# Performance work log

Hardware: AMD Instinct MI355X
Metric: run time of the kernel (lower is better)

## Reference

```python
import jax, jax.numpy as jnp
import numpy as np

B, C, H, W = 16, 64, 64, 64
HEADS = 8

def conv1x1(x, w):
    # x: [B, Cin, H, W], w: [Cout, Cin] -> [B, Cout, H, W]
    return jnp.einsum('oc,bchw->bohw', w, x)

def maxpool2x2(x):
    b, c, h, w = x.shape
    return x.reshape(b, c, h // 2, 2, w // 2, 2).max(axis=(3, 5))

def setup_inputs() -> dict:
    key = jax.random.key(0)
    ks = jax.random.split(key, 6)
    x = jax.random.normal(ks[0], (B, C, H, W), dtype=jnp.float32)
    w_theta = jax.random.normal(ks[1], (C // HEADS, C), dtype=jnp.float32) * 0.05
    w_phi = jax.random.normal(ks[2], (C // HEADS, C), dtype=jnp.float32) * 0.05
    w_g = jax.random.normal(ks[3], (C // 2, C), dtype=jnp.float32) * 0.05
    w_o = jax.random.normal(ks[4], (C, C // 2), dtype=jnp.float32) * 0.05
    gamma = jax.random.normal(ks[5], (), dtype=jnp.float32)
    return {'x': x, 'w_theta': w_theta, 'w_phi': w_phi, 'w_g': w_g, 'w_o': w_o, 'gamma': gamma}

def reference(x, w_theta, w_phi, w_g, w_o, gamma):
    b, c, h, w = x.shape
    n = h * w                      # query length
    m = n // 4                     # kv length after 2x2 maxpool
    theta = conv1x1(x, w_theta).reshape(b, c // HEADS, n)   # [B, C/h, N]
    phi = maxpool2x2(conv1x1(x, w_phi)).reshape(b, c // HEADS, m)  # [B, C/h, M]
    g = maxpool2x2(conv1x1(x, w_g)).reshape(b, c // 2, m)   # [B, C/2, M]
    # attention: theta^T @ phi -> [B, N, M]; NOTE: no 1/sqrt(d) scaling (SAGAN)
    beta = jax.nn.softmax(jnp.einsum('bdn,bdm->bnm', theta, phi), axis=-1)
    # o = g @ beta^T -> [B, C/2, N]
    o = jnp.einsum('bdm,bnm->bdn', g, beta).reshape(b, c // 2, h, w)
    o = conv1x1(o, w_o)            # [B, C, H, W]
    return gamma * o + x
```

## Files before the change

kernel.cpp:

```cpp
#include <hip/hip_runtime.h>
#include <hip/hip_bf16.h>

#define NB 16
#define NC 64
#define NN 4096
#define NM 1024
#define ND 8
#define NG 32

typedef short short8 __attribute__((ext_vector_type(8)));
typedef float floatx4 __attribute__((ext_vector_type(4)));

#define LOG2E 1.44269504f

__device__ __forceinline__ short f2bfs(float f) {
    union { __hip_bfloat16 h; short s; } u;
    u.h = __float2bfloat16(f);
    return u.s;
}
__device__ __forceinline__ unsigned pack2bf(float a, float b) {
    return (unsigned)(unsigned short)f2bfs(a) | ((unsigned)(unsigned short)f2bfs(b) << 16);
}
__device__ __forceinline__ unsigned pk2fast(float a, float b) {
    unsigned ua = __float_as_uint(a) + 0x8000u;
    unsigned ub = __float_as_uint(b) + 0x8000u;
    return __builtin_amdgcn_perm(ub, ua, 0x07060302);
}
__device__ __forceinline__ short8 u4s8(uint4 v) {
    union { uint4 u; short8 s; } c; c.u = v; return c.s;
}

__global__ __launch_bounds__(256)
void proj_kernel(const float* __restrict__ x,
                 const float* __restrict__ w_theta,
                 const float* __restrict__ w_phi,
                 const float* __restrict__ w_g,
                 const float* __restrict__ w_o,
                 unsigned* __restrict__ theta_ws,
                 unsigned* __restrict__ phi_ws,
                 unsigned* __restrict__ g2_ws)
{
    __shared__ __align__(16) float xl[64 * 128];
    __shared__ float lwt[512];
    __shared__ float lwp[512];
    __shared__ float lwg[2048];
    __shared__ float lwo[2048];
    __shared__ __align__(16) float lgs[32 * 36];
    __shared__ float lps[32 * 8];

    const int b  = blockIdx.x >> 5;
    const int ph = blockIdx.x & 31;
    const int t  = threadIdx.x;

    for (int i = t; i < 512;  i += 256) { lwt[i] = w_theta[i]; lwp[i] = w_phi[i]; }
    for (int i = t; i < 2048; i += 256) { lwg[i] = w_g[i];     lwo[i] = w_o[i]; }

    const float* xb = x + (size_t)b * NC * NN + (size_t)ph * 128;
    for (int idx = t; idx < 2048; idx += 256) {
        int c = idx >> 5, i4 = idx & 31;
        ((float4*)xl)[c * 32 + i4] = ((const float4*)(xb + (size_t)c * NN))[i4];
    }
    __syncthreads();

    if (t < 128) {
        float th[8];
        #pragma unroll
        for (int oc = 0; oc < 8; ++oc) th[oc] = 0.f;
        for (int c = 0; c < 64; ++c) {
            float xv = xl[c * 128 + t];
            #pragma unroll
            for (int oc = 0; oc < 8; ++oc) th[oc] = fmaf(lwt[oc * 64 + c], xv, th[oc]);
        }
        uint4 pk;
        pk.x = pack2bf(th[0] * LOG2E, th[1] * LOG2E);
        pk.y = pack2bf(th[2] * LOG2E, th[3] * LOG2E);
        pk.z = pack2bf(th[4] * LOG2E, th[5] * LOG2E);
        pk.w = pack2bf(th[6] * LOG2E, th[7] * LOG2E);
        ((uint4*)theta_ws)[(size_t)b * NN + ph * 128 + t] = pk;

        int m = t >> 2, oc0 = (t & 3) * 2;
        float s[2][4];
        #pragma unroll
        for (int a = 0; a < 2; ++a)
            #pragma unroll
            for (int p = 0; p < 4; ++p) s[a][p] = 0.f;
        #pragma unroll 4
        for (int c = 0; c < 64; ++c) {
            const float* xr = &xl[c * 128];
            float x0 = xr[2 * m], x1 = xr[2 * m + 1], x2 = xr[64 + 2 * m], x3 = xr[65 + 2 * m];
            #pragma unroll
            for (int a = 0; a < 2; ++a) {
                float w = lwp[(oc0 + a) * 64 + c];
                s[a][0] = fmaf(w, x0, s[a][0]);
                s[a][1] = fmaf(w, x1, s[a][1]);
                s[a][2] = fmaf(w, x2, s[a][2]);
                s[a][3] = fmaf(w, x3, s[a][3]);
            }
        }
        #pragma unroll
        for (int a = 0; a < 2; ++a)
            lps[m * 8 + oc0 + a] = fmaxf(fmaxf(s[a][0], s[a][1]), fmaxf(s[a][2], s[a][3]));
    } else {
        int tt = t - 128;
        int oc0 = (tt >> 3) * 2, grp = tt & 7;
        float s0[16], s1[16];
        #pragma unroll
        for (int i = 0; i < 16; ++i) { s0[i] = 0.f; s1[i] = 0.f; }
        const float4* xl4 = (const float4*)xl;
        #pragma unroll 2
        for (int c = 0; c < 64; ++c) {
            float4 a0 = xl4[c * 32 + 2 * grp];
            float4 a1 = xl4[c * 32 + 2 * grp + 1];
            float4 b0 = xl4[c * 32 + 16 + 2 * grp];
            float4 b1 = xl4[c * 32 + 17 + 2 * grp];
            float w0 = lwg[oc0 * 64 + c], w1 = lwg[(oc0 + 1) * 64 + c];
            s0[0] = fmaf(w0, a0.x, s0[0]);  s0[1] = fmaf(w0, a0.y, s0[1]);
            s0[2] = fmaf(w0, a0.z, s0[2]);  s0[3] = fmaf(w0, a0.w, s0[3]);
            s0[4] = fmaf(w0, a1.x, s0[4]);  s0[5] = fmaf(w0, a1.y, s0[5]);
            s0[6] = fmaf(w0, a1.z, s0[6]);  s0[7] = fmaf(w0, a1.w, s0[7]);
            s0[8] = fmaf(w0, b0.x, s0[8]);  s0[9] = fmaf(w0, b0.y, s0[9]);
            s0[10] = fmaf(w0, b0.z, s0[10]); s0[11] = fmaf(w0, b0.w, s0[11]);
            s0[12] = fmaf(w0, b1.x, s0[12]); s0[13] = fmaf(w0, b1.y, s0[13]);
            s0[14] = fmaf(w0, b1.z, s0[14]); s0[15] = fmaf(w0, b1.w, s0[15]);
            s1[0] = fmaf(w1, a0.x, s1[0]);  s1[1] = fmaf(w1, a0.y, s1[1]);
            s1[2] = fmaf(w1, a0.z, s1[2]);  s1[3] = fmaf(w1, a0.w, s1[3]);
            s1[4] = fmaf(w1, a1.x, s1[4]);  s1[5] = fmaf(w1, a1.y, s1[5]);
            s1[6] = fmaf(w1, a1.z, s1[6]);  s1[7] = fmaf(w1, a1.w, s1[7]);
            s1[8] = fmaf(w1, b0.x, s1[8]);  s1[9] = fmaf(w1, b0.y, s1[9]);
            s1[10] = fmaf(w1, b0.z, s1[10]); s1[11] = fmaf(w1, b0.w, s1[11]);
            s1[12] = fmaf(w1, b1.x, s1[12]); s1[13] = fmaf(w1, b1.y, s1[13]);
            s1[14] = fmaf(w1, b1.z, s1[14]); s1[15] = fmaf(w1, b1.w, s1[15]);
        }
        #pragma unroll
        for (int p = 0; p < 4; ++p) {
            float v0 = fmaxf(fmaxf(s0[2 * p], s0[2 * p + 1]), fmaxf(s0[8 + 2 * p], s0[9 + 2 * p]));
            float v1 = fmaxf(fmaxf(s1[2 * p], s1[2 * p + 1]), fmaxf(s1[8 + 2 * p], s1[9 + 2 * p]));
            lgs[oc0 * 36 + grp * 4 + p]       = v0;
            lgs[(oc0 + 1) * 36 + grp * 4 + p] = v1;
        }
    }
    __syncthreads();

    {
        int co = t >> 2, sel = t & 3;
        int m0a = 4 * sel, m0b = 16 + 4 * sel;
        float v[8];
        #pragma unroll
        for (int mm = 0; mm < 8; ++mm) v[mm] = 0.f;
        #pragma unroll 4
        for (int c = 0; c < 32; ++c) {
            float w = lwo[co * 32 + c];
            float4 ga = *(const float4*)&lgs[c * 36 + m0a];
            float4 gb = *(const float4*)&lgs[c * 36 + m0b];
            v[0] = fmaf(w, ga.x, v[0]); v[1] = fmaf(w, ga.y, v[1]);
            v[2] = fmaf(w, ga.z, v[2]); v[3] = fmaf(w, ga.w, v[3]);
            v[4] = fmaf(w, gb.x, v[4]); v[5] = fmaf(w, gb.y, v[5]);
            v[6] = fmaf(w, gb.z, v[6]); v[7] = fmaf(w, gb.w, v[7]);
        }
        uint4 pk;
        pk.x = pack2bf(v[0], v[1]); pk.y = pack2bf(v[2], v[3]);
        pk.z = pack2bf(v[4], v[5]); pk.w = pack2bf(v[6], v[7]);
        int lane = (sel << 4) | (co & 15);
        ((uint4*)g2_ws)[(((size_t)b * 4 + (co >> 4)) * 32 + ph) * 64 + lane] = pk;
    }

    if (t < 32) {
        const float* pr = &lps[t * 8];
        uint4 pk;
        pk.x = pack2bf(pr[0], pr[1]); pk.y = pack2bf(pr[2], pr[3]);
        pk.z = pack2bf(pr[4], pr[5]); pk.w = pack2bf(pr[6], pr[7]);
        ((uint4*)phi_ws)[(size_t)b * NM + ph * 32 + t] = pk;
    }
}

__global__ __launch_bounds__(256, 2)
void attn_kernel(const unsigned* __restrict__ theta_ws,
                 const unsigned* __restrict__ phi_ws,
                 const unsigned* __restrict__ g2_ws,
                 const float* __restrict__ gamma_p,
                 const float* __restrict__ x,
                 float* __restrict__ out)
{
    __shared__ __align__(16) uint4 lphi[NM];

    const int b    = blockIdx.x >> 5;
    const int qblk = blockIdx.x & 31;
    const int t    = threadIdx.x;
    const int w    = t >> 6;
    const int lane = t & 63;
    const int lm   = lane & 15;
    const int quad = lane >> 4;
    const int q0   = qblk * 128 + w * 32;

    for (int kk = t; kk < NM; kk += 256)
        lphi[kk] = ((const uint4*)phi_ws)[(size_t)b * NM + kk];

    uint4 tb[2];
    #pragma unroll
    for (int qt = 0; qt < 2; ++qt) {
        uint4 v = ((const uint4*)theta_ws)[(size_t)b * NN + q0 + qt * 16 + lm];
        tb[qt].x = quad == 0 ? v.x : 0u;
        tb[qt].y = quad == 0 ? v.y : 0u;
        tb[qt].z = quad == 0 ? v.z : 0u;
        tb[qt].w = quad == 0 ? v.w : 0u;
    }

    floatx4 acc[2][4];
    #pragma unroll
    for (int qt = 0; qt < 2; ++qt)
        #pragma unroll
        for (int ct = 0; ct < 4; ++ct) acc[qt][ct] = (floatx4)0.f;
    float lsum[2] = {0.f, 0.f};

    const uint4* gf = (const uint4*)g2_ws;
    uint4 ga[4], gn[4];
    #pragma unroll
    for (int ct = 0; ct < 4; ++ct)
        ga[ct] = gf[(((size_t)b * 4 + ct) * 32 + 0) * 64 + lane];

    __syncthreads();

    uint4 pp0 = lphi[lm];
    uint4 pp1 = lphi[16 + lm];

    for (int kg = 0; kg < 32; ++kg) {
        if (kg + 1 < 32) {
            #pragma unroll
            for (int ct = 0; ct < 4; ++ct)
                gn[ct] = gf[(((size_t)b * 4 + ct) * 32 + kg + 1) * 64 + lane];
        }
        uint4 pn0, pn1;
        if (kg + 1 < 32) {
            pn0 = lphi[(kg + 1) * 32 + lm];
            pn1 = lphi[(kg + 1) * 32 + 16 + lm];
        }

        #pragma unroll
        for (int qt = 0; qt < 2; ++qt) {
            floatx4 s0 = __builtin_amdgcn_mfma_f32_16x16x32_bf16(
                u4s8(pp0), u4s8(tb[qt]), (floatx4)0.f, 0, 0, 0);
            floatx4 s1 = __builtin_amdgcn_mfma_f32_16x16x32_bf16(
                u4s8(pp1), u4s8(tb[qt]), (floatx4)0.f, 0, 0, 0);
            float e0[4], e1[4];
            #pragma unroll
            for (int r = 0; r < 4; ++r) { e0[r] = exp2f(s0[r]); e1[r] = exp2f(s1[r]); }
            lsum[qt] += ((e0[0] + e0[1]) + (e0[2] + e0[3]))
                      + ((e1[0] + e1[1]) + (e1[2] + e1[3]));
            uint4 pb0 = make_uint4(pk2fast(e0[0], e0[1]), pk2fast(e0[2], e0[3]), 0u, 0u);
            uint4 pb1 = make_uint4(pk2fast(e1[0], e1[1]), pk2fast(e1[2], e1[3]), 0u, 0u);
            #pragma unroll
            for (int ct = 0; ct < 4; ++ct) {
                acc[qt][ct] = __builtin_amdgcn_mfma_f32_16x16x32_bf16(
                    u4s8(ga[ct]), u4s8(pb0), acc[qt][ct], 0, 0, 0);
                uint4 a1 = make_uint4(ga[ct].z, ga[ct].w, ga[ct].z, ga[ct].w);
                acc[qt][ct] = __builtin_amdgcn_mfma_f32_16x16x32_bf16(
                    u4s8(a1), u4s8(pb1), acc[qt][ct], 0, 0, 0);
            }
        }
        #pragma unroll
        for (int ct = 0; ct < 4; ++ct) ga[ct] = gn[ct];
        pp0 = pn0; pp1 = pn1;
    }

    float inv[2];
    {
        float l0 = lsum[0]; l0 += __shfl_xor(l0, 16); l0 += __shfl_xor(l0, 32);
        float l1 = lsum[1]; l1 += __shfl_xor(l1, 16); l1 += __shfl_xor(l1, 32);
        inv[0] = 1.0f / l0; inv[1] = 1.0f / l1;
    }

    const float gamma = gamma_p[0];
    #pragma unroll
    for (int qt = 0; qt < 2; ++qt) {
        const int q = q0 + qt * 16 + lm;
        #pragma unroll
        for (int ct = 0; ct < 4; ++ct) {
            #pragma unroll
            for (int r = 0; r < 4; ++r) {
                int co = ct * 16 + quad * 4 + r;
                size_t idx = ((size_t)b * NC + co) * NN + q;
                out[idx] = fmaf(gamma, acc[qt][ct][r] * inv[qt], x[idx]);
            }
        }
    }
}

extern "C" void kernel_launch(void* const* d_in, const int* in_sizes, int n_in,
                              void* d_out, int out_size, void* d_ws, size_t ws_size,
                              hipStream_t stream)
{
    const float* x  = (const float*)d_in[0];
    const float* wt = (const float*)d_in[1];
    const float* wp = (const float*)d_in[2];
    const float* wg = (const float*)d_in[3];
    const float* wo = (const float*)d_in[4];
    const float* gm = (const float*)d_in[5];
    float* out = (float*)d_out;

    unsigned* theta_ws = (unsigned*)d_ws;
    unsigned* phi_ws   = theta_ws + (size_t)NB * NN * ND / 2;
    unsigned* g2_ws    = phi_ws   + (size_t)NB * NM * ND / 2;

    proj_kernel<<<NB * 32, 256, 0, stream>>>(x, wt, wp, wg, wo, theta_ws, phi_ws, g2_ws);
    attn_kernel<<<NB * 32, 256, 0, stream>>>(theta_ws, phi_ws, g2_ws, gm, x, out);
}
```

Baseline: 121.2 us.

## Stage attention epilogue through LDS for vectorized stores; double-buffer kv prefetch

The attention epilogue now writes normalized accumulators into a padded LDS tile and re-reads them so that x loads and out stores are coalesced float4 accesses, replacing scattered scalar global accesses. The kv loop is unrolled by two with A/B register buffers, so the g and phi loads for a step are issued two iterations ahead, and it uses the raw exp2 intrinsic. In the projection kernel the w_g and w_o weights are stored transposed and padded in LDS, which lets w_g be read as a float2 and avoids bank conflicts. These changes add LDS traffic, two barriers and more register pressure in exchange for better memory coalescing and latency hiding.

```diff
diff --git a/kernel.cpp b/kernel.cpp
--- a/kernel.cpp
+++ b/kernel.cpp
@@ -43,8 +43,8 @@
     __shared__ __align__(16) float xl[64 * 128];
     __shared__ float lwt[512];
     __shared__ float lwp[512];
-    __shared__ float lwg[2048];
-    __shared__ float lwo[2048];
+    __shared__ __align__(8) float lwgT[64 * 34];
+    __shared__ float lwoT[32 * 65];
     __shared__ __align__(16) float lgs[32 * 36];
     __shared__ float lps[32 * 8];
 
@@ -53,7 +53,10 @@
     const int t  = threadIdx.x;
 
     for (int i = t; i < 512;  i += 256) { lwt[i] = w_theta[i]; lwp[i] = w_phi[i]; }
-    for (int i = t; i < 2048; i += 256) { lwg[i] = w_g[i];     lwo[i] = w_o[i]; }
+    for (int i = t; i < 2048; i += 256) {
+        lwgT[(i & 63) * 34 + (i >> 6)] = w_g[i];
+        lwoT[(i & 31) * 65 + (i >> 5)] = w_o[i];
+    }
 
     const float* xb = x + (size_t)b * NC * NN + (size_t)ph * 128;
     for (int idx = t; idx < 2048; idx += 256) {
@@ -113,7 +116,8 @@
             float4 a1 = xl4[c * 32 + 2 * grp + 1];
             float4 b0 = xl4[c * 32 + 16 + 2 * grp];
             float4 b1 = xl4[c * 32 + 17 + 2 * grp];
-            float w0 = lwg[oc0 * 64 + c], w1 = lwg[(oc0 + 1) * 64 + c];
+            float2 wv = *(const float2*)&lwgT[c * 34 + oc0];
+            float w0 = wv.x, w1 = wv.y;
             s0[0] = fmaf(w0, a0.x, s0[0]);  s0[1] = fmaf(w0, a0.y, s0[1]);
             s0[2] = fmaf(w0, a0.z, s0[2]);  s0[3] = fmaf(w0, a0.w, s0[3]);
             s0[4] = fmaf(w0, a1.x, s0[4]);  s0[5] = fmaf(w0, a1.y, s0[5]);
@@ -149,7 +153,7 @@
         for (int mm = 0; mm < 8; ++mm) v[mm] = 0.f;
         #pragma unroll 4
         for (int c = 0; c < 32; ++c) {
-            float w = lwo[co * 32 + c];
+            float w = lwoT[c * 65 + co];
             float4 ga = *(const float4*)&lgs[c * 36 + m0a];
             float4 gb = *(const float4*)&lgs[c * 36 + m0b];
             v[0] = fmaf(w, ga.x, v[0]); v[1] = fmaf(w, ga.y, v[1]);
@@ -172,6 +176,35 @@
         ((uint4*)phi_ws)[(size_t)b * NM + ph * 32 + t] = pk;
     }
 }
+
+#define KG_STEP(CPP0, CPP1, CG)                                                          \
+    {                                                                                    \
+        _Pragma("unroll")                                                                \
+        for (int qt = 0; qt < 2; ++qt) {                                                 \
+            floatx4 s0 = __builtin_amdgcn_mfma_f32_16x16x32_bf16(                        \
+                u4s8(CPP0), u4s8(tb[qt]), (floatx4)0.f, 0, 0, 0);                        \
+            floatx4 s1 = __builtin_amdgcn_mfma_f32_16x16x32_bf16(                        \
+                u4s8(CPP1), u4s8(tb[qt]), (floatx4)0.f, 0, 0, 0);                        \
+            float e0[4], e1[4];                                                          \
+            _Pragma("unroll")                                                            \
+            for (int r = 0; r < 4; ++r) {                                                \
+                e0[r] = __builtin_amdgcn_exp2f(s0[r]);                                   \
+                e1[r] = __builtin_amdgcn_exp2f(s1[r]);                                   \
+            }                                                                            \
+            lsum[qt] += ((e0[0] + e0[1]) + (e0[2] + e0[3]))                              \
+                      + ((e1[0] + e1[1]) + (e1[2] + e1[3]));                             \
+            uint4 pq0 = make_uint4(pk2fast(e0[0], e0[1]), pk2fast(e0[2], e0[3]), 0u, 0u);\
+            uint4 pq1 = make_uint4(pk2fast(e1[0], e1[1]), pk2fast(e1[2], e1[3]), 0u, 0u);\
+            _Pragma("unroll")                                                            \
+            for (int ct = 0; ct < 4; ++ct) {                                             \
+                acc[qt][ct] = __builtin_amdgcn_mfma_f32_16x16x32_bf16(                   \
+                    u4s8(CG[ct]), u4s8(pq0), acc[qt][ct], 0, 0, 0);                      \
+                uint4 a1 = make_uint4(CG[ct].z, CG[ct].w, CG[ct].z, CG[ct].w);           \
+                acc[qt][ct] = __builtin_amdgcn_mfma_f32_16x16x32_bf16(                   \
+                    u4s8(a1), u4s8(pq1), acc[qt][ct], 0, 0, 0);                          \
+            }                                                                            \
+        }                                                                                \
+    }
 
 __global__ __launch_bounds__(256, 2)
 void attn_kernel(const unsigned* __restrict__ theta_ws,
@@ -181,7 +214,9 @@
                  const float* __restrict__ x,
                  float* __restrict__ out)
 {
-    __shared__ __align__(16) uint4 lphi[NM];
+    __shared__ __align__(16) float smem_f[64 * 140];
+    uint4* lphi = (uint4*)smem_f;
+    float* ltr  = smem_f;
 
     const int b    = blockIdx.x >> 5;
     const int qblk = blockIdx.x & 31;
@@ -213,53 +248,45 @@
     float lsum[2] = {0.f, 0.f};
 
     const uint4* gf = (const uint4*)g2_ws;
-    uint4 ga[4], gn[4];
+    uint4 gA[4], gB[4];
     #pragma unroll
-    for (int ct = 0; ct < 4; ++ct)
-        ga[ct] = gf[(((size_t)b * 4 + ct) * 32 + 0) * 64 + lane];
-
-    __syncthreads();
-
-    uint4 pp0 = lphi[lm];
-    uint4 pp1 = lphi[16 + lm];
-
-    for (int kg = 0; kg < 32; ++kg) {
-        if (kg + 1 < 32) {
-            #pragma unroll
-            for (int ct = 0; ct < 4; ++ct)
-                gn[ct] = gf[(((size_t)b * 4 + ct) * 32 + kg + 1) * 64 + lane];
-        }
-        uint4 pn0, pn1;
-        if (kg + 1 < 32) {
-            pn0 = lphi[(kg + 1) * 32 + lm];
-            pn1 = lphi[(kg + 1) * 32 + 16 + lm];
-        }
-
-        #pragma unroll
-        for (int qt = 0; qt < 2; ++qt) {
-            floatx4 s0 = __builtin_amdgcn_mfma_f32_16x16x32_bf16(
-                u4s8(pp0), u4s8(tb[qt]), (floatx4)0.f, 0, 0, 0);
-            floatx4 s1 = __builtin_amdgcn_mfma_f32_16x16x32_bf16(
-                u4s8(pp1), u4s8(tb[qt]), (floatx4)0.f, 0, 0, 0);
-            float e0[4], e1[4];
-            #pragma unroll
-            for (int r = 0; r < 4; ++r) { e0[r] = exp2f(s0[r]); e1[r] = exp2f(s1[r]); }
-            lsum[qt] += ((e0[0] + e0[1]) + (e0[2] + e0[3]))
-                      + ((e1[0] + e1[1]) + (e1[2] + e1[3]));
-            uint4 pb0 = make_uint4(pk2fast(e0[0], e0[1]), pk2fast(e0[2], e0[3]), 0u, 0u);
-            uint4 pb1 = make_uint4(pk2fast(e1[0], e1[1]), pk2fast(e1[2], e1[3]), 0u, 0u);
-            #pragma unroll
-            for (int ct = 0; ct < 4; ++ct) {
-                acc[qt][ct] = __builtin_amdgcn_mfma_f32_16x16x32_bf16(
-                    u4s8(ga[ct]), u4s8(pb0), acc[qt][ct], 0, 0, 0);
-                uint4 a1 = make_uint4(ga[ct].z, ga[ct].w, ga[ct].z, ga[ct].w);
-                acc[qt][ct] = __builtin_amdgcn_mfma_f32_16x16x32_bf16(
-                    u4s8(a1), u4s8(pb1), acc[qt][ct], 0, 0, 0);
+    for (int ct = 0; ct < 4; ++ct) {
+        gA[ct] = gf[(((size_t)b * 4 + ct) * 32 + 0) * 64 + lane];
+        gB[ct] = gf[(((size_t)b * 4 + ct) * 32 + 1) * 64 + lane];
+    }
+
+    __syncthreads();
+
+    uint4 qA0 = lphi[lm],      qA1 = lphi[16 + lm];
+    uint4 qB0 = lphi[32 + lm], qB1 = lphi[48 + lm];
+
+    for (int kg2 = 0; kg2 < 16; ++kg2) {
+        {
+            uint4 c0 = qA0, c1 = qA1;
+            uint4 cg[4] = {gA[0], gA[1], gA[2], gA[3]};
+            if (kg2 < 15) {
+                int nk = 2 * kg2 + 2;
+                qA0 = lphi[nk * 32 + lm];
+                qA1 = lphi[nk * 32 + 16 + lm];
+                #pragma unroll
+                for (int ct = 0; ct < 4; ++ct)
+                    gA[ct] = gf[(((size_t)b * 4 + ct) * 32 + nk) * 64 + lane];
             }
-        }
-        #pragma unroll
-        for (int ct = 0; ct < 4; ++ct) ga[ct] = gn[ct];
-        pp0 = pn0; pp1 = pn1;
+            KG_STEP(c0, c1, cg);
+        }
+        {
+            uint4 c0 = qB0, c1 = qB1;
+            uint4 cg[4] = {gB[0], gB[1], gB[2], gB[3]};
+            if (kg2 < 15) {
+                int nk = 2 * kg2 + 3;
+                qB0 = lphi[nk * 32 + lm];
+                qB1 = lphi[nk * 32 + 16 + lm];
+                #pragma unroll
+                for (int ct = 0; ct < 4; ++ct)
+                    gB[ct] = gf[(((size_t)b * 4 + ct) * 32 + nk) * 64 + lane];
+            }
+            KG_STEP(c0, c1, cg);
+        }
     }
 
     float inv[2];
@@ -270,17 +297,35 @@
     }
 
     const float gamma = gamma_p[0];
+
+    __syncthreads();
     #pragma unroll
-    for (int qt = 0; qt < 2; ++qt) {
-        const int q = q0 + qt * 16 + lm;
-        #pragma unroll
-        for (int ct = 0; ct < 4; ++ct) {
+    for (int qt = 0; qt < 2; ++qt)
+        #pragma unroll
+        for (int ct = 0; ct < 4; ++ct)
             #pragma unroll
-            for (int r = 0; r < 4; ++r) {
-                int co = ct * 16 + quad * 4 + r;
-                size_t idx = ((size_t)b * NC + co) * NN + q;
-                out[idx] = fmaf(gamma, acc[qt][ct][r] * inv[qt], x[idx]);
-            }
+            for (int r = 0; r < 4; ++r)
+                ltr[(ct * 16 + quad * 4 + r) * 140 + w * 32 + qt * 16 + lm]
+                    = acc[qt][ct][r] * inv[qt];
+    __syncthreads();
+
+    {
+        const int l16 = t & 15;
+        #pragma unroll
+        for (int io = 0; io < 4; ++io) {
+            int co = io * 16 + (t >> 4);
+            size_t base = ((size_t)b * NC + co) * NN + qblk * 128 + l16 * 8;
+            const float* tr = &ltr[co * 140 + l16 * 8];
+            float4 t0 = ((const float4*)tr)[0];
+            float4 t1 = ((const float4*)tr)[1];
+            float4 x0 = *(const float4*)(x + base);
+            float4 x1 = *(const float4*)(x + base + 4);
+            float4 o0 = make_float4(fmaf(gamma, t0.x, x0.x), fmaf(gamma, t0.y, x0.y),
+                                    fmaf(gamma, t0.z, x0.z), fmaf(gamma, t0.w, x0.w));
+            float4 o1 = make_float4(fmaf(gamma, t1.x, x1.x), fmaf(gamma, t1.y, x1.y),
+                                    fmaf(gamma, t1.z, x1.z), fmaf(gamma, t1.w, x1.w));
+            *(float4*)(out + base)     = o0;
+            *(float4*)(out + base + 4) = o1;
         }
     }
 }
```

Result: faster. 113.3 us (-6.5%).
